# Kernel optimization log

Measured on AMD Instinct MI355X. Metric: run time of the kernel, lower is better.

Reference implementation:

```python
import jax, jax.numpy as jnp
import numpy as np

N_NODES = 10000
AVG_DEG = 16
N_EDGES = N_NODES * AVG_DEG
NODE_DIM, EDGE_DIM, LIN_DIM, HID, OUT, LAYERS = 9, 3, 32, 300, 2, 5


def _init(key, shape, fan_in):
    return jax.random.normal(key, shape, jnp.float32) * (1.0 / np.sqrt(fan_in))


def setup_inputs() -> dict:
    key = jax.random.key(0)
    ks = jax.random.split(key, 18)
    inp = {
        "x": jax.random.normal(ks[0], (N_NODES, NODE_DIM), jnp.float32),
        "edge_index": jax.random.randint(ks[1], (2, N_EDGES), 0, N_NODES, jnp.int32),
        "edge_attr": jax.random.normal(ks[2], (N_EDGES, EDGE_DIM), jnp.float32),
        "batch": jnp.zeros((N_NODES,), jnp.int32),
        # nn.Linear params (stored as [in, out] so fwd is x @ W + b)
        "node_w": _init(ks[3], (NODE_DIM, LIN_DIM), NODE_DIM),
        "node_b": jnp.zeros((LIN_DIM,), jnp.float32),
        "edge_w": _init(ks[4], (EDGE_DIM, LIN_DIM), EDGE_DIM),
        "edge_b": jnp.zeros((LIN_DIM,), jnp.float32),
        # GCNConv: lin (no bias) + separate additive bias (PyG convention)
        "gcn0_w": _init(ks[5], (LIN_DIM, HID), LIN_DIM),
        "gcn0_b": jnp.zeros((HID,), jnp.float32),
        "gcn_w": _init(ks[6], (LAYERS - 1, HID, HID), HID),
        "gcn_b": jnp.zeros((LAYERS - 1, HID), jnp.float32),
        "lin1_w": _init(ks[7], (HID, LIN_DIM), HID),
        "lin1_b": jnp.zeros((LIN_DIM,), jnp.float32),
        "lin2_w": _init(ks[8], (LIN_DIM, OUT), LIN_DIM),
        "lin2_b": jnp.zeros((OUT,), jnp.float32),
    }
    return inp


def reference(x, edge_index, edge_attr, batch,
              node_w, node_b, edge_w, edge_b,
              gcn0_w, gcn0_b, gcn_w, gcn_b,
              lin1_w, lin1_b, lin2_w, lin2_b):
    row, col = edge_index[0], edge_index[1]

    e = edge_attr @ edge_w + edge_b  # [E, LIN_DIM] edge embeddings

    # Faithful to the original bug: node embeddings get edge attrs scatter-added,
    # then the result is discarded by `attr = edge_attr`. Kept for fidelity (dead).
    node_h = x @ node_w + node_b
    node_h = node_h.at[row].add(e)  # unused downstream

    # GCN stack runs over the E-row edge-embedding matrix -> effective node count = E
    h = e
    n = h.shape[0]  # == N_EDGES

    # symmetric gcn_norm with self-loops (edge_weight = 1), computed once
    deg = jax.ops.segment_sum(jnp.ones((edge_index.shape[1],), h.dtype), col,
                              num_segments=n) + 1.0
    dinv = jax.lax.rsqrt(deg)
    norm = dinv[row] * dinv[col]  # per-edge normalization
    self_norm = (dinv * dinv)[:, None]  # self-loop term

    def gcn(h, w, b):
        hw = h @ w  # dense transform
        agg = jax.ops.segment_sum(hw[row] * norm[:, None], col, num_segments=n)
        return agg + self_norm * hw + b

    h = jax.nn.relu(gcn(h, gcn0_w, gcn0_b))

    def step(h, wb):
        w, b = wb
        return jax.nn.relu(gcn(h, w, b)), None

    h, _ = jax.lax.scan(step, h, (gcn_w, gcn_b))

    g = jnp.mean(h, axis=0, keepdims=True)  # [1, HID] graph readout
    g = jax.nn.relu(g @ lin1_w + lin1_b)
    pred = g @ lin2_w + lin2_b  # [1, OUT]; forward returns pre-softmax logits
    return pred
```

## Files before the change

### kernel.cpp

```cpp
#include <hip/hip_runtime.h>
#include <hip/hip_bf16.h>

#define N_NODES 10000
#define N_EDGES 160000
#define HID 300
#define HIDP 304
#define NPARTB (N_EDGES - N_NODES)
#define KS 328
#define RBM 80
#define RBF 32
#define PARTB_BLOCKS 1875
#define GEMMA_BLOCKS 125
#define FILL_BLOCKS 313
#define MEGA_BLOCKS (PARTB_BLOCKS + GEMMA_BLOCKS + FILL_BLOCKS)
#define FUSE_BLOCKS 313

typedef __attribute__((ext_vector_type(8))) short short8;
typedef __attribute__((ext_vector_type(4))) float f32x4;

#define MFMA_B16(a, b, c) __builtin_amdgcn_mfma_f32_16x16x32_bf16(a, b, c, 0, 0, 0)

__device__ __forceinline__ short bf16r(float x) {
    unsigned u = __float_as_uint(x);
    return (short)((u + 0x7fffu + ((u >> 16) & 1u)) >> 16);
}
__device__ __forceinline__ float b2f(unsigned short u) {
    return __uint_as_float(((unsigned)u) << 16);
}
__device__ __forceinline__ void split1(float x, short& hi, short& lo) {
    short h = bf16r(x);
    float hf = __uint_as_float(((unsigned)(unsigned short)h) << 16);
    hi = h;
    lo = bf16r(x - hf);
}

__global__ void k_prep(const float* __restrict__ g0w, const float* __restrict__ gw,
                       short* __restrict__ wt0, short* __restrict__ wtl,
                       const int* __restrict__ col, int* __restrict__ cnt) {
    int idx = blockIdx.x * 256 + threadIdx.x;
    if (idx < N_EDGES) atomicAdd(&cnt[col[idx]], 1);
    if (idx < 1216) {
        int n16 = idx & 15, q = (idx >> 4) & 3, nt = idx >> 6;
        int n = nt * 16 + n16;
        short* hd = wt0 + (size_t)(nt * 8 + q) * 128 + n16 * 8;
        short* ld = wt0 + (size_t)(nt * 8 + 4 + q) * 128 + n16 * 8;
#pragma unroll
        for (int j = 0; j < 8; ++j) {
            int k = q * 8 + j;
            float f = (n < HID) ? g0w[k * HID + n] : 0.0f;
            short hi, lo;
            split1(f, hi, lo);
            hd[j] = hi;
            ld[j] = lo;
        }
    } else if (idx < 1216 + 48640) {
        int i = idx - 1216;
        int n16 = i & 15; i >>= 4;
        int q = i & 3; i >>= 2;
        int nt = i % 19; i /= 19;
        int chunk = i % 10;
        int l = i / 10;
        int n = nt * 16 + n16;
        int cnt_idx = chunk * 19 + nt;
        short* base = wtl + (size_t)l * 194560;
        short* hd = base + (size_t)(cnt_idx * 8 + q) * 128 + n16 * 8;
        short* ld = base + (size_t)(cnt_idx * 8 + 4 + q) * 128 + n16 * 8;
#pragma unroll
        for (int j = 0; j < 8; ++j) {
            int k = chunk * 32 + q * 8 + j;
            float f = (k < HID && n < HID) ? gw[((size_t)l * HID + k) * HID + n] : 0.0f;
            short hi, lo;
            split1(f, hi, lo);
            hd[j] = hi;
            ld[j] = lo;
        }
    }
}

__global__ __launch_bounds__(1024) void k_scan(
    const int* __restrict__ cnt, int* __restrict__ col_start,
    int* __restrict__ cursor, float* __restrict__ dinv,
    float* __restrict__ selfnorm) {
    __shared__ int wsum[16];
    int t = threadIdx.x;
    int lane = t & 63, w = t >> 6;
    int carry = 0;
    for (int base = 0; base < N_NODES; base += 1024) {
        int i = base + t;
        int v = (i < N_NODES) ? cnt[i] : 0;
        int s = v;
#pragma unroll
        for (int d = 1; d < 64; d <<= 1) {
            int n = __shfl_up(s, d, 64);
            if (lane >= d) s += n;
        }
        if (lane == 63) wsum[w] = s;
        __syncthreads();
        int woff = 0, total = 0;
#pragma unroll
        for (int k = 0; k < 16; ++k) {
            if (k < w) woff += wsum[k];
            total += wsum[k];
        }
        if (i < N_NODES) {
            int excl = carry + woff + s - v;
            col_start[i] = excl;
            cursor[i] = excl;
            float dd = (float)v + 1.0f;
            dinv[i] = rsqrtf(dd);
            selfnorm[i] = 1.0f / dd;
        }
        carry += total;
        __syncthreads();
    }
    if (t == 0) col_start[N_NODES] = carry;
}

template <int MT, int NTC>
__device__ __forceinline__ void kloop(const short* __restrict__ wp, int nch,
                                      const short* Hh, int nt0, int quad, int l16,
                                      f32x4 (&acc)[MT][NTC]) {
#pragma unroll
    for (int mt = 0; mt < MT; ++mt)
#pragma unroll
        for (int i = 0; i < NTC; ++i)
#pragma unroll
            for (int r = 0; r < 4; ++r) acc[mt][i][r] = 0.0f;
#pragma unroll 1
    for (int c = 0; c < nch; ++c) {
        const short* cb = wp + (size_t)(c * 19 + nt0) * 1024 + quad * 128 + l16 * 8;
        short8 ah[MT];
#pragma unroll
        for (int mt = 0; mt < MT; ++mt)
            ah[mt] = *(const short8*)&Hh[(mt * 16 + l16) * KS + c * 32 + quad * 8];
        short8 bb[NTC];
#pragma unroll
        for (int i = 0; i < NTC; ++i) bb[i] = *(const short8*)(cb + (size_t)i * 1024);
#pragma unroll
        for (int mt = 0; mt < MT; ++mt)
#pragma unroll
            for (int i = 0; i < NTC; ++i)
                acc[mt][i] = MFMA_B16(ah[mt], bb[i], acc[mt][i]);
#pragma unroll
        for (int i = 0; i < NTC; ++i) bb[i] = *(const short8*)(cb + (size_t)i * 1024 + 512);
#pragma unroll
        for (int mt = 0; mt < MT; ++mt)
#pragma unroll
            for (int i = 0; i < NTC; ++i)
                acc[mt][i] = MFMA_B16(ah[mt], bb[i], acc[mt][i]);
    }
}

template <int MT, int NTC>
__device__ __forceinline__ void gcn_epilogue(const float* __restrict__ bias,
                                             int nt0, int quad, int l16,
                                             f32x4 (&acc)[MT][NTC], short* Hh) {
#pragma unroll
    for (int i = 0; i < NTC; ++i) {
        int c = (nt0 + i) * 16 + l16;
        float b = (c < HID) ? bias[c] : 0.0f;
#pragma unroll
        for (int mt = 0; mt < MT; ++mt)
#pragma unroll
            for (int r = 0; r < 4; ++r) {
                float v = fmaxf(acc[mt][i][r] + b, 0.0f);
                Hh[(mt * 16 + quad * 4 + r) * KS + c] = bf16r(v);
            }
    }
}

template <int MT, int NTC>
__device__ __forceinline__ void gcn_final(const float* __restrict__ bias,
                                          int nt0, int quad, int l16,
                                          f32x4 (&acc)[MT][NTC],
                                          float* __restrict__ gout) {
#pragma unroll
    for (int i = 0; i < NTC; ++i) {
        int c = (nt0 + i) * 16 + l16;
        float b = (c < HID) ? bias[c] : 0.0f;
        float s = 0.0f;
#pragma unroll
        for (int mt = 0; mt < MT; ++mt)
#pragma unroll
            for (int r = 0; r < 4; ++r) s += fmaxf(acc[mt][i][r] + b, 0.0f);
        s += __shfl_xor(s, 16, 64);
        s += __shfl_xor(s, 32, 64);
        if (quad == 0) gout[c] = (c < HID) ? s : 0.0f;
    }
}

template <int MT, int NTC>
__device__ __forceinline__ void gemm_out(int base, int nt0, int quad, int l16,
                                         f32x4 (&acc)[MT][NTC],
                                         unsigned short* __restrict__ HW) {
#pragma unroll
    for (int i = 0; i < NTC; ++i) {
        int c = (nt0 + i) * 16 + l16;
#pragma unroll
        for (int mt = 0; mt < MT; ++mt)
#pragma unroll
            for (int r = 0; r < 4; ++r) {
                int gm = base + mt * 16 + quad * 4 + r;
                if (gm < N_NODES)
                    HW[(size_t)gm * HIDP + c] = (unsigned short)bf16r(acc[mt][i][r]);
            }
    }
}

__global__ __launch_bounds__(512, 4) void k_mega(
    const float* __restrict__ edge_attr,
    const float* __restrict__ edge_w,
    const float* __restrict__ edge_b,
    const short* __restrict__ wt0,
    const short* __restrict__ wtl,
    const float* __restrict__ gcn0_b,
    const float* __restrict__ gcn_b,
    float* __restrict__ gpartB,
    unsigned short* __restrict__ hw0,
    const int* __restrict__ row,
    const int* __restrict__ col,
    int* __restrict__ cursor,
    const float* __restrict__ dinv,
    int2* __restrict__ edge_pack) {
    __shared__ short Hh[RBM * KS];
    int bid = blockIdx.x, t = threadIdx.x;
    int lane = t & 63, w = t >> 6;
    int l16 = lane & 15, quad = lane >> 4;
    int nt0 = (w < 3) ? w * 3 : 9 + (w - 3) * 2;

    if (bid < PARTB_BLOCKS) {
        int base = N_NODES + bid * RBM;
        for (int i = t; i < RBM * 8; i += 512) {
            int r = i >> 3, c4 = (i & 7) * 4;
            const float* ar = edge_attr + (size_t)(base + r) * 3;
            float a0 = ar[0], a1 = ar[1], a2 = ar[2];
#pragma unroll
            for (int j = 0; j < 4; ++j) {
                int cc = c4 + j;
                float v = edge_b[cc];
                v = fmaf(a0, edge_w[cc], v);
                v = fmaf(a1, edge_w[32 + cc], v);
                v = fmaf(a2, edge_w[64 + cc], v);
                Hh[r * KS + cc] = bf16r(v);
            }
        }
        for (int i = t; i < RBM * 24; i += 512) {
            int r = i / 24, k = 304 + i % 24;
            Hh[r * KS + k] = 0;
        }
        __syncthreads();

        float* gout = gpartB + (size_t)bid * HIDP;
        if (w < 3) {
            f32x4 acc[5][3];
            kloop<5, 3>(wt0, 1, Hh, nt0, quad, l16, acc);
            __syncthreads();
            gcn_epilogue<5, 3>(gcn0_b, nt0, quad, l16, acc, Hh);
            __syncthreads();
            for (int l = 0; l < 4; ++l) {
                kloop<5, 3>(wtl + (size_t)l * 194560, 10, Hh, nt0, quad, l16, acc);
                __syncthreads();
                if (l < 3) {
                    gcn_epilogue<5, 3>(gcn_b + l * HID, nt0, quad, l16, acc, Hh);
                    __syncthreads();
                } else {
                    gcn_final<5, 3>(gcn_b + l * HID, nt0, quad, l16, acc, gout);
                }
            }
        } else {
            f32x4 acc[5][2];
            kloop<5, 2>(wt0, 1, Hh, nt0, quad, l16, acc);
            __syncthreads();
            gcn_epilogue<5, 2>(gcn0_b, nt0, quad, l16, acc, Hh);
            __syncthreads();
            for (int l = 0; l < 4; ++l) {
                kloop<5, 2>(wtl + (size_t)l * 194560, 10, Hh, nt0, quad, l16, acc);
                __syncthreads();
                if (l < 3) {
                    gcn_epilogue<5, 2>(gcn_b + l * HID, nt0, quad, l16, acc, Hh);
                    __syncthreads();
                } else {
                    gcn_final<5, 2>(gcn_b + l * HID, nt0, quad, l16, acc, gout);
                }
            }
        }
    } else if (bid < PARTB_BLOCKS + GEMMA_BLOCKS) {
        int base = (bid - PARTB_BLOCKS) * RBM;
        for (int i = t; i < RBM * 8; i += 512) {
            int r = i >> 3, c4 = (i & 7) * 4;
            const float* ar = edge_attr + (size_t)(base + r) * 3;
            float a0 = ar[0], a1 = ar[1], a2 = ar[2];
#pragma unroll
            for (int j = 0; j < 4; ++j) {
                int cc = c4 + j;
                float v = edge_b[cc];
                v = fmaf(a0, edge_w[cc], v);
                v = fmaf(a1, edge_w[32 + cc], v);
                v = fmaf(a2, edge_w[64 + cc], v);
                Hh[r * KS + cc] = bf16r(v);
            }
        }
        for (int i = t; i < RBM * 24; i += 512) {
            int r = i / 24, k = 304 + i % 24;
            Hh[r * KS + k] = 0;
        }
        __syncthreads();
        if (w < 3) {
            f32x4 acc[5][3];
            kloop<5, 3>(wt0, 1, Hh, nt0, quad, l16, acc);
            gemm_out<5, 3>(base, nt0, quad, l16, acc, hw0);
        } else {
            f32x4 acc[5][2];
            kloop<5, 2>(wt0, 1, Hh, nt0, quad, l16, acc);
            gemm_out<5, 2>(base, nt0, quad, l16, acc, hw0);
        }
    } else {
        int e = (bid - PARTB_BLOCKS - GEMMA_BLOCKS) * 512 + t;
        if (e < N_EDGES) {
            int c = col[e], r = row[e];
            int p = atomicAdd(&cursor[c], 1);
            edge_pack[p] = make_int2(r, __float_as_int(dinv[r] * dinv[c]));
        }
    }
}

__device__ __forceinline__ void agg_row(int c, int lane,
                                        const unsigned short* __restrict__ hw_in,
                                        const int* __restrict__ col_start,
                                        const int2* __restrict__ edge_pack,
                                        float (&v)[5]) {
#pragma unroll
    for (int jj = 0; jj < 5; ++jj) v[jj] = 0.0f;
    int beg = col_start[c], end = col_start[c + 1];
    int i = beg;
    for (; i + 4 <= end; i += 4) {
        int2 e0 = edge_pack[i], e1 = edge_pack[i + 1];
        int2 e2 = edge_pack[i + 2], e3 = edge_pack[i + 3];
        const unsigned short* h0 = hw_in + (size_t)e0.x * HIDP;
        const unsigned short* h1 = hw_in + (size_t)e1.x * HIDP;
        const unsigned short* h2 = hw_in + (size_t)e2.x * HIDP;
        const unsigned short* h3 = hw_in + (size_t)e3.x * HIDP;
        float n0 = __int_as_float(e0.y), n1 = __int_as_float(e1.y);
        float n2 = __int_as_float(e2.y), n3 = __int_as_float(e3.y);
#pragma unroll
        for (int jj = 0; jj < 5; ++jj) {
            int cc = lane + 64 * jj;
            if (cc < HIDP) {
                float s = v[jj];
                s = fmaf(n0, b2f(h0[cc]), s);
                s = fmaf(n1, b2f(h1[cc]), s);
                s = fmaf(n2, b2f(h2[cc]), s);
                s = fmaf(n3, b2f(h3[cc]), s);
                v[jj] = s;
            }
        }
    }
    for (; i < end; ++i) {
        int2 e0 = edge_pack[i];
        const unsigned short* h0 = hw_in + (size_t)e0.x * HIDP;
        float n0 = __int_as_float(e0.y);
#pragma unroll
        for (int jj = 0; jj < 5; ++jj) {
            int cc = lane + 64 * jj;
            if (cc < HIDP) v[jj] = fmaf(n0, b2f(h0[cc]), v[jj]);
        }
    }
}

__global__ __launch_bounds__(512, 6) void k_fuse(
    const unsigned short* __restrict__ hw_in,
    const int* __restrict__ col_start,
    const int2* __restrict__ edge_pack,
    const float* __restrict__ selfnorm,
    const float* __restrict__ bias,
    const short* __restrict__ wt,
    unsigned short* __restrict__ hw_out) {
    __shared__ short Hh[RBF * KS];
    int t = threadIdx.x;
    int lane = t & 63, w = t >> 6;
    int l16 = lane & 15, quad = lane >> 4;
    int base = blockIdx.x * RBF;
    int nt0 = (w < 3) ? w * 3 : 9 + (w - 3) * 2;

#pragma unroll 1
    for (int j = 0; j < 4; ++j) {
        int r = w * 4 + j;
        int c = base + r;
        if (c < N_NODES) {
            float v[5];
            agg_row(c, lane, hw_in, col_start, edge_pack, v);
            float sn = selfnorm[c];
            const unsigned short* sp = hw_in + (size_t)c * HIDP;
#pragma unroll
            for (int jj = 0; jj < 5; ++jj) {
                int cc = lane + 64 * jj;
                if (cc < HIDP) {
                    float h = v[jj] + sn * b2f(sp[cc]) + ((cc < HID) ? bias[cc] : 0.0f);
                    Hh[r * KS + cc] = bf16r(fmaxf(h, 0.0f));
                }
            }
        } else {
#pragma unroll
            for (int jj = 0; jj < 5; ++jj) {
                int cc = lane + 64 * jj;
                if (cc < HIDP) Hh[r * KS + cc] = 0;
            }
        }
    }
    for (int i = t; i < RBF * 24; i += 512) {
        int r = i / 24, k = 304 + i % 24;
        Hh[r * KS + k] = 0;
    }
    __syncthreads();

    if (w < 3) {
        f32x4 acc[2][3];
        kloop<2, 3>(wt, 10, Hh, nt0, quad, l16, acc);
        gemm_out<2, 3>(base, nt0, quad, l16, acc, hw_out);
    } else {
        f32x4 acc[2][2];
        kloop<2, 2>(wt, 10, Hh, nt0, quad, l16, acc);
        gemm_out<2, 2>(base, nt0, quad, l16, acc, hw_out);
    }
}

__global__ __launch_bounds__(512) void k_last(
    const unsigned short* __restrict__ hw_in,
    const int* __restrict__ col_start,
    const int2* __restrict__ edge_pack,
    const float* __restrict__ selfnorm,
    const float* __restrict__ bias,
    const float* __restrict__ gpartB,
    float* __restrict__ g_sum) {
    __shared__ float red[8 * 320];
    int t = threadIdx.x;
    int lane = t & 63, w = t >> 6;
    int base = blockIdx.x * RBF;

    float s[5] = {0.0f, 0.0f, 0.0f, 0.0f, 0.0f};
#pragma unroll 1
    for (int j = 0; j < 4; ++j) {
        int c = base + w * 4 + j;
        if (c < N_NODES) {
            float v[5];
            agg_row(c, lane, hw_in, col_start, edge_pack, v);
            float sn = selfnorm[c];
            const unsigned short* sp = hw_in + (size_t)c * HIDP;
#pragma unroll
            for (int jj = 0; jj < 5; ++jj) {
                int cc = lane + 64 * jj;
                if (cc < HID) {
                    float h = v[jj] + sn * b2f(sp[cc]) + bias[cc];
                    s[jj] += fmaxf(h, 0.0f);
                }
            }
        }
    }
    if (w < 6) {
        int rr = blockIdx.x * 6 + w;
        if (rr < PARTB_BLOCKS) {
#pragma unroll
            for (int jj = 0; jj < 5; ++jj) {
                int cc = lane + 64 * jj;
                if (cc < HID) s[jj] += gpartB[(size_t)rr * HIDP + cc];
            }
        }
    }
#pragma unroll
    for (int jj = 0; jj < 5; ++jj) red[w * 320 + lane + 64 * jj] = s[jj];
    __syncthreads();
    if (w == 0) {
#pragma unroll
        for (int jj = 0; jj < 5; ++jj) {
            int cc = lane + 64 * jj;
            if (cc < HID) {
                float tot = 0.0f;
#pragma unroll
                for (int g = 0; g < 8; ++g) tot += red[g * 320 + cc];
                atomicAdd(&g_sum[cc], tot);
            }
        }
    }
}

__global__ void k_head(const float* __restrict__ g_sum,
                       const float* __restrict__ lin1_w, const float* __restrict__ lin1_b,
                       const float* __restrict__ lin2_w, const float* __restrict__ lin2_b,
                       float* __restrict__ out) {
    __shared__ float g2[32];
    int t = threadIdx.x;
    const float inv = 1.0f / (float)N_EDGES;
    if (t < 32) {
        float a = lin1_b[t];
        for (int d = 0; d < HID; ++d) a = fmaf(g_sum[d] * inv, lin1_w[d * 32 + t], a);
        g2[t] = fmaxf(a, 0.0f);
    }
    __syncthreads();
    if (t < 2) {
        float p = lin2_b[t];
        for (int j = 0; j < 32; ++j) p = fmaf(g2[j], lin2_w[j * 2 + t], p);
        out[t] = p;
    }
}


extern "C" void kernel_launch(void* const* d_in, const int* in_sizes, int n_in,
                              void* d_out, int out_size, void* d_ws, size_t ws_size,
                              hipStream_t stream) {
    (void)in_sizes; (void)n_in; (void)out_size; (void)ws_size;
    const int* edge_index = (const int*)d_in[1];
    const float* edge_attr = (const float*)d_in[2];
    const float* edge_w = (const float*)d_in[6];
    const float* edge_b = (const float*)d_in[7];
    const float* gcn0_w = (const float*)d_in[8];
    const float* gcn0_b = (const float*)d_in[9];
    const float* gcn_w = (const float*)d_in[10];
    const float* gcn_b = (const float*)d_in[11];
    const float* lin1_w = (const float*)d_in[12];
    const float* lin1_b = (const float*)d_in[13];
    const float* lin2_w = (const float*)d_in[14];
    const float* lin2_b = (const float*)d_in[15];

    char* ws = (char*)d_ws;
    size_t off = 0;
    auto alloc = [&](size_t bytes) {
        void* p = ws + off;
        off = (off + bytes + 255) & ~(size_t)255;
        return p;
    };
    unsigned short* hwA = (unsigned short*)alloc((size_t)N_NODES * HIDP * 2);
    unsigned short* hwB = (unsigned short*)alloc((size_t)N_NODES * HIDP * 2);
    int2* edge_pack = (int2*)alloc((size_t)N_EDGES * 8);
    int* cnt = (int*)alloc((size_t)N_NODES * 4);
    int* col_start = (int*)alloc((size_t)(N_NODES + 1) * 4);
    int* cursor = (int*)alloc((size_t)N_NODES * 4);
    float* dinv = (float*)alloc((size_t)N_NODES * 4);
    float* selfnorm = (float*)alloc((size_t)N_NODES * 4);
    float* g_sum = (float*)alloc((size_t)HIDP * 4);
    short* wt0 = (short*)alloc((size_t)38912);
    short* wtl = (short*)alloc((size_t)4 * 389120);
    float* gpartB = (float*)alloc((size_t)PARTB_BLOCKS * HIDP * 4);

    const int* row = edge_index;
    const int* col = edge_index + N_EDGES;

    hipMemsetAsync(cnt, 0, N_NODES * 4, stream);
    hipMemsetAsync(g_sum, 0, HIDP * 4, stream);

    k_prep<<<(N_EDGES + 255) / 256, 256, 0, stream>>>(gcn0_w, gcn_w, wt0, wtl, col, cnt);
    k_scan<<<1, 1024, 0, stream>>>(cnt, col_start, cursor, dinv, selfnorm);

    k_mega<<<MEGA_BLOCKS, 512, 0, stream>>>(edge_attr, edge_w, edge_b, wt0, wtl,
                                            gcn0_b, gcn_b, gpartB, hwA,
                                            row, col, cursor, dinv, edge_pack);

    k_fuse<<<FUSE_BLOCKS, 512, 0, stream>>>(hwA, col_start, edge_pack, selfnorm,
                                            gcn0_b, wtl + (size_t)0 * 194560, hwB);
    k_fuse<<<FUSE_BLOCKS, 512, 0, stream>>>(hwB, col_start, edge_pack, selfnorm,
                                            gcn_b + 0 * HID, wtl + (size_t)1 * 194560, hwA);
    k_fuse<<<FUSE_BLOCKS, 512, 0, stream>>>(hwA, col_start, edge_pack, selfnorm,
                                            gcn_b + 1 * HID, wtl + (size_t)2 * 194560, hwB);
    k_fuse<<<FUSE_BLOCKS, 512, 0, stream>>>(hwB, col_start, edge_pack, selfnorm,
                                            gcn_b + 2 * HID, wtl + (size_t)3 * 194560, hwA);
    k_last<<<FUSE_BLOCKS, 512, 0, stream>>>(hwA, col_start, edge_pack, selfnorm,
                                            gcn_b + 3 * HID, gpartB, g_sum);
    k_head<<<1, 64, 0, stream>>>(g_sum, lin1_w, lin1_b, lin2_w, lin2_b, (float*)d_out);
}
```

Before: 467.1 us.

## Halve fuse row tile, software-pipeline MFMA k-loop, widen gather unroll

Halves the rows per block in the fused aggregate+GEMM and last-layer kernels (16 instead of 32) and doubles the grid, so more blocks spread across CUs. It software-pipelines the MFMA k-loop by prefetching the next chunk's A and B fragments while the current ones are multiplied. It also adds an 8-edge unrolled gather path in agg_row and relaxes the occupancy hints in launch_bounds. In exchange, each weight fragment loaded from global memory is reused across fewer rows, the prefetch buffers raise register pressure, and the removal of the N_NODES bounds checks relies on 10000 dividing evenly by 16.

```diff
diff --git a/kernel.cpp b/kernel.cpp
--- a/kernel.cpp
+++ b/kernel.cpp
@@ -8,14 +8,15 @@
 #define NPARTB (N_EDGES - N_NODES)
 #define KS 328
 #define RBM 80
-#define RBF 32
+#define RBF 16
 #define PARTB_BLOCKS 1875
 #define GEMMA_BLOCKS 125
 #define FILL_BLOCKS 313
 #define MEGA_BLOCKS (PARTB_BLOCKS + GEMMA_BLOCKS + FILL_BLOCKS)
-#define FUSE_BLOCKS 313
+#define FUSE_BLOCKS 625
 
 typedef __attribute__((ext_vector_type(8))) short short8;
+typedef __attribute__((ext_vector_type(4))) short s16x4;
 typedef __attribute__((ext_vector_type(4))) float f32x4;
 
 #define MFMA_B16(a, b, c) __builtin_amdgcn_mfma_f32_16x16x32_bf16(a, b, c, 0, 0, 0)
@@ -126,28 +127,52 @@
         for (int i = 0; i < NTC; ++i)
 #pragma unroll
             for (int r = 0; r < 4; ++r) acc[mt][i][r] = 0.0f;
+
+    const short* a0 = Hh + l16 * KS + quad * 8;
+    const short* w0 = wp + (size_t)nt0 * 1024 + (size_t)(quad * 128 + l16 * 8);
+
+    short8 ah[MT], an[MT], b1[NTC], b1n[NTC], b2[NTC];
+#pragma unroll
+    for (int mt = 0; mt < MT; ++mt) ah[mt] = *(const short8*)(a0 + mt * 16 * KS);
+#pragma unroll
+    for (int i = 0; i < NTC; ++i) b1[i] = *(const short8*)(w0 + (size_t)i * 1024);
+
 #pragma unroll 1
-    for (int c = 0; c < nch; ++c) {
-        const short* cb = wp + (size_t)(c * 19 + nt0) * 1024 + quad * 128 + l16 * 8;
-        short8 ah[MT];
+    for (int c = 0; c < nch - 1; ++c) {
+        const short* wc = w0 + (size_t)c * 19456;
+        const short* wn = wc + 19456;
+        const short* apn = a0 + (c + 1) * 32;
+#pragma unroll
+        for (int i = 0; i < NTC; ++i) b2[i] = *(const short8*)(wc + (size_t)i * 1024 + 512);
+#pragma unroll
+        for (int mt = 0; mt < MT; ++mt) an[mt] = *(const short8*)(apn + mt * 16 * KS);
+#pragma unroll
+        for (int i = 0; i < NTC; ++i) b1n[i] = *(const short8*)(wn + (size_t)i * 1024);
 #pragma unroll
         for (int mt = 0; mt < MT; ++mt)
-            ah[mt] = *(const short8*)&Hh[(mt * 16 + l16) * KS + c * 32 + quad * 8];
-        short8 bb[NTC];
-#pragma unroll
-        for (int i = 0; i < NTC; ++i) bb[i] = *(const short8*)(cb + (size_t)i * 1024);
+#pragma unroll
+            for (int i = 0; i < NTC; ++i) acc[mt][i] = MFMA_B16(ah[mt], b1[i], acc[mt][i]);
 #pragma unroll
         for (int mt = 0; mt < MT; ++mt)
 #pragma unroll
-            for (int i = 0; i < NTC; ++i)
-                acc[mt][i] = MFMA_B16(ah[mt], bb[i], acc[mt][i]);
-#pragma unroll
-        for (int i = 0; i < NTC; ++i) bb[i] = *(const short8*)(cb + (size_t)i * 1024 + 512);
+            for (int i = 0; i < NTC; ++i) acc[mt][i] = MFMA_B16(ah[mt], b2[i], acc[mt][i]);
+#pragma unroll
+        for (int mt = 0; mt < MT; ++mt) ah[mt] = an[mt];
+#pragma unroll
+        for (int i = 0; i < NTC; ++i) b1[i] = b1n[i];
+    }
+    {
+        const short* wc = w0 + (size_t)(nch - 1) * 19456;
+#pragma unroll
+        for (int i = 0; i < NTC; ++i) b2[i] = *(const short8*)(wc + (size_t)i * 1024 + 512);
 #pragma unroll
         for (int mt = 0; mt < MT; ++mt)
 #pragma unroll
-            for (int i = 0; i < NTC; ++i)
-                acc[mt][i] = MFMA_B16(ah[mt], bb[i], acc[mt][i]);
+            for (int i = 0; i < NTC; ++i) acc[mt][i] = MFMA_B16(ah[mt], b1[i], acc[mt][i]);
+#pragma unroll
+        for (int mt = 0; mt < MT; ++mt)
+#pragma unroll
+            for (int i = 0; i < NTC; ++i) acc[mt][i] = MFMA_B16(ah[mt], b2[i], acc[mt][i]);
     }
 }
 
@@ -207,7 +232,7 @@
     }
 }
 
-__global__ __launch_bounds__(512, 4) void k_mega(
+__global__ __launch_bounds__(512, 3) void k_mega(
     const float* __restrict__ edge_attr,
     const float* __restrict__ edge_w,
     const float* __restrict__ edge_b,
@@ -333,6 +358,42 @@
     for (int jj = 0; jj < 5; ++jj) v[jj] = 0.0f;
     int beg = col_start[c], end = col_start[c + 1];
     int i = beg;
+#pragma unroll 1
+    for (; i + 8 <= end; i += 8) {
+        int2 e0 = edge_pack[i], e1 = edge_pack[i + 1];
+        int2 e2 = edge_pack[i + 2], e3 = edge_pack[i + 3];
+        int2 e4 = edge_pack[i + 4], e5 = edge_pack[i + 5];
+        int2 e6 = edge_pack[i + 6], e7 = edge_pack[i + 7];
+        const unsigned short* h0 = hw_in + (size_t)e0.x * HIDP;
+        const unsigned short* h1 = hw_in + (size_t)e1.x * HIDP;
+        const unsigned short* h2 = hw_in + (size_t)e2.x * HIDP;
+        const unsigned short* h3 = hw_in + (size_t)e3.x * HIDP;
+        const unsigned short* h4 = hw_in + (size_t)e4.x * HIDP;
+        const unsigned short* h5 = hw_in + (size_t)e5.x * HIDP;
+        const unsigned short* h6 = hw_in + (size_t)e6.x * HIDP;
+        const unsigned short* h7 = hw_in + (size_t)e7.x * HIDP;
+        float n0 = __int_as_float(e0.y), n1 = __int_as_float(e1.y);
+        float n2 = __int_as_float(e2.y), n3 = __int_as_float(e3.y);
+        float n4 = __int_as_float(e4.y), n5 = __int_as_float(e5.y);
+        float n6 = __int_as_float(e6.y), n7 = __int_as_float(e7.y);
+#pragma unroll
+        for (int jj = 0; jj < 5; ++jj) {
+            int cc = lane + 64 * jj;
+            if (cc < HIDP) {
+                float s = v[jj];
+                s = fmaf(n0, b2f(h0[cc]), s);
+                s = fmaf(n1, b2f(h1[cc]), s);
+                s = fmaf(n2, b2f(h2[cc]), s);
+                s = fmaf(n3, b2f(h3[cc]), s);
+                s = fmaf(n4, b2f(h4[cc]), s);
+                s = fmaf(n5, b2f(h5[cc]), s);
+                s = fmaf(n6, b2f(h6[cc]), s);
+                s = fmaf(n7, b2f(h7[cc]), s);
+                v[jj] = s;
+            }
+        }
+    }
+#pragma unroll 1
     for (; i + 4 <= end; i += 4) {
         int2 e0 = edge_pack[i], e1 = edge_pack[i + 1];
         int2 e2 = edge_pack[i + 2], e3 = edge_pack[i + 3];
@@ -355,6 +416,7 @@
             }
         }
     }
+#pragma unroll 1
     for (; i < end; ++i) {
         int2 e0 = edge_pack[i];
         const unsigned short* h0 = hw_in + (size_t)e0.x * HIDP;
@@ -367,7 +429,7 @@
     }
 }
 
-__global__ __launch_bounds__(512, 6) void k_fuse(
+__global__ __launch_bounds__(512, 4) void k_fuse(
     const unsigned short* __restrict__ hw_in,
     const int* __restrict__ col_start,
     const int2* __restrict__ edge_pack,
@@ -383,44 +445,36 @@
     int nt0 = (w < 3) ? w * 3 : 9 + (w - 3) * 2;
 
 #pragma unroll 1
-    for (int j = 0; j < 4; ++j) {
-        int r = w * 4 + j;
+    for (int j = 0; j < 2; ++j) {
+        int r = w * 2 + j;
         int c = base + r;
-        if (c < N_NODES) {
-            float v[5];
-            agg_row(c, lane, hw_in, col_start, edge_pack, v);
-            float sn = selfnorm[c];
-            const unsigned short* sp = hw_in + (size_t)c * HIDP;
-#pragma unroll
-            for (int jj = 0; jj < 5; ++jj) {
-                int cc = lane + 64 * jj;
-                if (cc < HIDP) {
-                    float h = v[jj] + sn * b2f(sp[cc]) + ((cc < HID) ? bias[cc] : 0.0f);
-                    Hh[r * KS + cc] = bf16r(fmaxf(h, 0.0f));
-                }
-            }
-        } else {
-#pragma unroll
-            for (int jj = 0; jj < 5; ++jj) {
-                int cc = lane + 64 * jj;
-                if (cc < HIDP) Hh[r * KS + cc] = 0;
-            }
-        }
-    }
-    for (int i = t; i < RBF * 24; i += 512) {
-        int r = i / 24, k = 304 + i % 24;
-        Hh[r * KS + k] = 0;
+        float v[5];
+        agg_row(c, lane, hw_in, col_start, edge_pack, v);
+        float sn = selfnorm[c];
+        const unsigned short* sp = hw_in + (size_t)c * HIDP;
+#pragma unroll
+        for (int jj = 0; jj < 5; ++jj) {
+            int cc = lane + 64 * jj;
+            if (cc < HIDP) {
+                float h = v[jj] + sn * b2f(sp[cc]) + ((cc < HID) ? bias[cc] : 0.0f);
+                Hh[r * KS + cc] = bf16r(fmaxf(h, 0.0f));
+            }
+        }
+    }
+    for (int i = t; i < RBF * 6; i += 512) {
+        int r = i / 6, k = 304 + (i % 6) * 4;
+        *(s16x4*)&Hh[r * KS + k] = (s16x4)0;
     }
     __syncthreads();
 
     if (w < 3) {
-        f32x4 acc[2][3];
-        kloop<2, 3>(wt, 10, Hh, nt0, quad, l16, acc);
-        gemm_out<2, 3>(base, nt0, quad, l16, acc, hw_out);
+        f32x4 acc[1][3];
+        kloop<1, 3>(wt, 10, Hh, nt0, quad, l16, acc);
+        gemm_out<1, 3>(base, nt0, quad, l16, acc, hw_out);
     } else {
-        f32x4 acc[2][2];
-        kloop<2, 2>(wt, 10, Hh, nt0, quad, l16, acc);
-        gemm_out<2, 2>(base, nt0, quad, l16, acc, hw_out);
+        f32x4 acc[1][2];
+        kloop<1, 2>(wt, 10, Hh, nt0, quad, l16, acc);
+        gemm_out<1, 2>(base, nt0, quad, l16, acc, hw_out);
     }
 }
 
@@ -439,25 +493,23 @@
 
     float s[5] = {0.0f, 0.0f, 0.0f, 0.0f, 0.0f};
 #pragma unroll 1
-    for (int j = 0; j < 4; ++j) {
-        int c = base + w * 4 + j;
-        if (c < N_NODES) {
-            float v[5];
-            agg_row(c, lane, hw_in, col_start, edge_pack, v);
-            float sn = selfnorm[c];
-            const unsigned short* sp = hw_in + (size_t)c * HIDP;
-#pragma unroll
-            for (int jj = 0; jj < 5; ++jj) {
-                int cc = lane + 64 * jj;
-                if (cc < HID) {
-                    float h = v[jj] + sn * b2f(sp[cc]) + bias[cc];
-                    s[jj] += fmaxf(h, 0.0f);
-                }
-            }
-        }
-    }
-    if (w < 6) {
-        int rr = blockIdx.x * 6 + w;
+    for (int j = 0; j < 2; ++j) {
+        int c = base + w * 2 + j;
+        float v[5];
+        agg_row(c, lane, hw_in, col_start, edge_pack, v);
+        float sn = selfnorm[c];
+        const unsigned short* sp = hw_in + (size_t)c * HIDP;
+#pragma unroll
+        for (int jj = 0; jj < 5; ++jj) {
+            int cc = lane + 64 * jj;
+            if (cc < HID) {
+                float h = v[jj] + sn * b2f(sp[cc]) + bias[cc];
+                s[jj] += fmaxf(h, 0.0f);
+            }
+        }
+    }
+    if (w < 3) {
+        int rr = blockIdx.x * 3 + w;
         if (rr < PARTB_BLOCKS) {
 #pragma unroll
             for (int jj = 0; jj < 5; ++jj) {
```

Result: slower. 492.9 us (+5.5%).
